# Kernel tuning notes

Measured on AMD Instinct MI355X. Metric: run time of the kernel, lower is better.

The kernel has to match this reference:

```python
import jax, jax.numpy as jnp
import numpy as np

D_MODEL = 1024
NUM_HEADS = 16
HEAD_DIM = D_MODEL // NUM_HEADS
D_FF = 4096
BATCH = 4
SEQ = 2048
LN_EPS = 1e-6
NEG_INF = -1e10


def setup_inputs() -> dict:
    key = jax.random.key(0)
    ks = jax.random.split(key, 8)
    def lin_init(k, fan_in, fan_out):
        # flax default: lecun_normal kernel, zeros bias
        w = jax.random.normal(k, (fan_in, fan_out), jnp.float32) / np.sqrt(fan_in)
        b = jnp.zeros((fan_out,), jnp.float32)
        return w, b
    x = jax.random.normal(ks[0], (BATCH, SEQ, D_MODEL), jnp.float32)
    w_qkv, b_qkv = lin_init(ks[1], D_MODEL, 3 * D_MODEL)
    w_out, b_out = lin_init(ks[2], D_MODEL, D_MODEL)
    w_fc1, b_fc1 = lin_init(ks[3], D_MODEL, D_FF)
    w_fc2, b_fc2 = lin_init(ks[4], D_FF, D_MODEL)
    ln1_scale = jnp.ones((D_MODEL,), jnp.float32)
    ln1_bias = jnp.zeros((D_MODEL,), jnp.float32)
    ln2_scale = jnp.ones((D_MODEL,), jnp.float32)
    ln2_bias = jnp.zeros((D_MODEL,), jnp.float32)
    return {
        'x': x,
        'w_qkv': w_qkv, 'b_qkv': b_qkv,
        'w_out': w_out, 'b_out': b_out,
        'w_fc1': w_fc1, 'b_fc1': b_fc1,
        'w_fc2': w_fc2, 'b_fc2': b_fc2,
        'ln1_scale': ln1_scale, 'ln1_bias': ln1_bias,
        'ln2_scale': ln2_scale, 'ln2_bias': ln2_bias,
    }


def _layernorm(x, scale, bias):
    mu = jnp.mean(x, axis=-1, keepdims=True)
    var = jnp.mean(jnp.square(x - mu), axis=-1, keepdims=True)
    return (x - mu) * jax.lax.rsqrt(var + LN_EPS) * scale + bias


def _attention(x, w_qkv, b_qkv, w_out, b_out):
    B, S, _ = x.shape
    qkv = x @ w_qkv + b_qkv                      # [B,S,3*D]
    qkv = qkv.reshape(B, S, 3, NUM_HEADS, HEAD_DIM)
    q, k, v = qkv[:, :, 0], qkv[:, :, 1], qkv[:, :, 2]   # [B,S,H,D]
    q = q.transpose(0, 2, 1, 3)                  # [B,H,S,D]
    k = k.transpose(0, 2, 1, 3)
    v = v.transpose(0, 2, 1, 3)
    scores = jnp.einsum('bhqd,bhkd->bhqk', q, k) / np.sqrt(HEAD_DIM)
    causal = jnp.tril(jnp.ones((S, S), bool))[None, None]
    scores = jnp.where(causal, scores, NEG_INF)
    attn = jax.nn.softmax(scores, axis=-1)
    out = jnp.einsum('bhqk,bhkd->bhqd', attn, v)  # [B,H,S,D]
    out = out.transpose(0, 2, 1, 3).reshape(B, S, D_MODEL)
    return out @ w_out + b_out


def _mlp(x, w_fc1, b_fc1, w_fc2, b_fc2):
    h = jax.nn.gelu(x @ w_fc1 + b_fc1)  # approximate (tanh) gelu, matching nnx.gelu default
    return h @ w_fc2 + b_fc2


def reference(x, w_qkv, b_qkv, w_out, b_out, w_fc1, b_fc1, w_fc2, b_fc2,
              ln1_scale, ln1_bias, ln2_scale, ln2_bias):
    x = x + _attention(_layernorm(x, ln1_scale, ln1_bias), w_qkv, b_qkv, w_out, b_out)
    x = x + _mlp(_layernorm(x, ln2_scale, ln2_bias), w_fc1, b_fc1, w_fc2, b_fc2)
    return x
```

## Files before the change

### kernel.cpp

```cpp
#include <hip/hip_runtime.h>

typedef unsigned short u16;
typedef unsigned int u32;
typedef __bf16 bf16x8 __attribute__((ext_vector_type(8)));
typedef float f32x4 __attribute__((ext_vector_type(4)));

constexpr int SEQ = 2048;

__device__ __forceinline__ float bf2f(u16 u) {
    u32 x = ((u32)u) << 16;
    return __builtin_bit_cast(float, x);
}
__device__ __forceinline__ u16 f2bf(float f) {
    u32 u = __builtin_bit_cast(u32, f);
    u32 r = u + 0x7fffu + ((u >> 16) & 1u);
    return (u16)(r >> 16);
}
__device__ __forceinline__ u32 cvt_pk_bf16(float a, float b) {
    u32 d;
    asm("v_cvt_pk_bf16_f32 %0, %1, %2" : "=v"(d) : "v"(a), "v"(b));
    return d;
}
__device__ __forceinline__ bf16x8 ld_frag(const u16* p) {
    uint4 u = *(const uint4*)p;
    return __builtin_bit_cast(bf16x8, u);
}
__device__ __forceinline__ float gelu_f(float x) {
    float u = 0.7978845608028654f * (x + 0.044715f * x * x * x);
    float e = exp2f(u * 2.885390081777927f);
    float t = 1.f - 2.f / (1.f + e);
    return 0.5f * x * (1.f + t);
}
__device__ __forceinline__ bool probe_f32(const u32* p) { return (p[0] & 0xFFFFu) == 0u; }

__device__ __forceinline__ void load_lds16(const u16* g, u16* l) {
    __builtin_amdgcn_global_load_lds(
        (const __attribute__((address_space(1))) void*)g,
        (__attribute__((address_space(3))) void*)l, 16, 0, 0);
}

__global__ __launch_bounds__(256) void convert_to_bf16(const void* __restrict__ in, long long off,
                                                       u16* __restrict__ out, int n,
                                                       const u32* __restrict__ probe) {
    const bool f32 = probe_f32(probe);
    int i = (blockIdx.x * 256 + threadIdx.x) * 4;
    if (i >= n) return;
    if (f32) {
        const float4 v = *(const float4*)((const float*)in + off + i);
        uint2 o;
        o.x = (u32)f2bf(v.x) | ((u32)f2bf(v.y) << 16);
        o.y = (u32)f2bf(v.z) | ((u32)f2bf(v.w) << 16);
        *(uint2*)(out + i) = o;
    } else {
        *(uint2*)(out + i) = *(const uint2*)((const u16*)in + off + i);
    }
}

__global__ __launch_bounds__(256) void finalize_out(const u16* __restrict__ in, void* __restrict__ outv,
                                                    long long off, int n, const u32* __restrict__ probe) {
    const bool f32 = probe_f32(probe);
    int i = (blockIdx.x * 256 + threadIdx.x) * 4;
    if (i >= n) return;
    uint2 v = *(const uint2*)(in + i);
    if (f32) {
        float4 o;
        o.x = bf2f((u16)(v.x & 0xffffu));
        o.y = bf2f((u16)(v.x >> 16));
        o.z = bf2f((u16)(v.y & 0xffffu));
        o.w = bf2f((u16)(v.y >> 16));
        *(float4*)((float*)outv + off + i) = o;
    } else {
        *(uint2*)((u16*)outv + off + i) = v;
    }
}

__global__ __launch_bounds__(256) void transpose_any(const void* __restrict__ in,
                                                     u16* __restrict__ out,
                                                     int K, int N, const u32* __restrict__ probe) {
    const bool f32 = probe_f32(probe);
    __shared__ u16 tile[32][33];
    int tx = threadIdx.x & 31, ty = threadIdx.x >> 5;
    int k0 = blockIdx.y * 32, n0 = blockIdx.x * 32;
    for (int i = 0; i < 32; i += 8) {
        size_t idx = (size_t)(k0 + ty + i) * N + n0 + tx;
        tile[ty + i][tx] = f32 ? f2bf(((const float*)in)[idx]) : ((const u16*)in)[idx];
    }
    __syncthreads();
    for (int i = 0; i < 32; i += 8)
        out[(size_t)(n0 + ty + i) * K + k0 + tx] = tile[tx][ty + i];
}

__global__ __launch_bounds__(256) void fused_cvt_ln(const void* __restrict__ xraw, long long off,
                                                    const u16* __restrict__ sc,
                                                    const u16* __restrict__ bi,
                                                    u16* __restrict__ xbf,
                                                    u16* __restrict__ xn,
                                                    const u32* __restrict__ probe) {
    const bool f32 = probe_f32(probe);
    int row = blockIdx.x;
    int tid = threadIdx.x;
    float v[4];
    if (f32) {
        const float4 q = *(const float4*)((const float*)xraw + off + (size_t)row * 1024 + tid * 4);
        v[0] = q.x; v[1] = q.y; v[2] = q.z; v[3] = q.w;
    } else {
        uint2 u = *(const uint2*)((const u16*)xraw + off + (size_t)row * 1024 + tid * 4);
        v[0] = bf2f((u16)(u.x & 0xffffu)); v[1] = bf2f((u16)(u.x >> 16));
        v[2] = bf2f((u16)(u.y & 0xffffu)); v[3] = bf2f((u16)(u.y >> 16));
    }
    {
        uint2 c;
        c.x = (u32)f2bf(v[0]) | ((u32)f2bf(v[1]) << 16);
        c.y = (u32)f2bf(v[2]) | ((u32)f2bf(v[3]) << 16);
        *(uint2*)(xbf + (size_t)row * 1024 + tid * 4) = c;
    }
    float s1 = 0.f, s2 = 0.f;
    for (int i = 0; i < 4; i++) { s1 += v[i]; s2 += v[i] * v[i]; }
    for (int off2 = 32; off2 >= 1; off2 >>= 1) {
        s1 += __shfl_xor(s1, off2, 64);
        s2 += __shfl_xor(s2, off2, 64);
    }
    __shared__ float red[8];
    int wave = tid >> 6, lane = tid & 63;
    if (lane == 0) { red[wave] = s1; red[4 + wave] = s2; }
    __syncthreads();
    s1 = red[0] + red[1] + red[2] + red[3];
    s2 = red[4] + red[5] + red[6] + red[7];
    float mean = s1 * (1.f / 1024.f);
    float var = s2 * (1.f / 1024.f) - mean * mean;
    float rstd = rsqrtf(var + 1e-6f);
    int c = tid * 4;
    float y0 = (v[0] - mean) * rstd * bf2f(sc[c + 0]) + bf2f(bi[c + 0]);
    float y1 = (v[1] - mean) * rstd * bf2f(sc[c + 1]) + bf2f(bi[c + 1]);
    float y2 = (v[2] - mean) * rstd * bf2f(sc[c + 2]) + bf2f(bi[c + 2]);
    float y3 = (v[3] - mean) * rstd * bf2f(sc[c + 3]) + bf2f(bi[c + 3]);
    uint2 ov;
    ov.x = (u32)f2bf(y0) | ((u32)f2bf(y1) << 16);
    ov.y = (u32)f2bf(y2) | ((u32)f2bf(y3) << 16);
    *(uint2*)(xn + (size_t)row * 1024 + tid * 4) = ov;
}

__global__ __launch_bounds__(256) void layernorm_k(const u16* __restrict__ x,
                                                   const u16* __restrict__ sc,
                                                   const u16* __restrict__ bi,
                                                   u16* __restrict__ out) {
    int row = blockIdx.x;
    int tid = threadIdx.x;
    const u16* xr = x + (size_t)row * 1024;
    uint2 u = *(const uint2*)(xr + tid * 4);
    float v[4];
    v[0] = bf2f((u16)(u.x & 0xffffu));
    v[1] = bf2f((u16)(u.x >> 16));
    v[2] = bf2f((u16)(u.y & 0xffffu));
    v[3] = bf2f((u16)(u.y >> 16));
    float s1 = 0.f, s2 = 0.f;
    for (int i = 0; i < 4; i++) { s1 += v[i]; s2 += v[i] * v[i]; }
    for (int off = 32; off >= 1; off >>= 1) {
        s1 += __shfl_xor(s1, off, 64);
        s2 += __shfl_xor(s2, off, 64);
    }
    __shared__ float red[8];
    int wave = tid >> 6, lane = tid & 63;
    if (lane == 0) { red[wave] = s1; red[4 + wave] = s2; }
    __syncthreads();
    s1 = red[0] + red[1] + red[2] + red[3];
    s2 = red[4] + red[5] + red[6] + red[7];
    float mean = s1 * (1.f / 1024.f);
    float var = s2 * (1.f / 1024.f) - mean * mean;
    float rstd = rsqrtf(var + 1e-6f);
    u32 o0, o1;
    {
        int c = tid * 4;
        float y0 = (v[0] - mean) * rstd * bf2f(sc[c + 0]) + bf2f(bi[c + 0]);
        float y1 = (v[1] - mean) * rstd * bf2f(sc[c + 1]) + bf2f(bi[c + 1]);
        float y2 = (v[2] - mean) * rstd * bf2f(sc[c + 2]) + bf2f(bi[c + 2]);
        float y3 = (v[3] - mean) * rstd * bf2f(sc[c + 3]) + bf2f(bi[c + 3]);
        o0 = (u32)f2bf(y0) | ((u32)f2bf(y1) << 16);
        o1 = (u32)f2bf(y2) | ((u32)f2bf(y3) << 16);
    }
    uint2 ov; ov.x = o0; ov.y = o1;
    *(uint2*)(out + (size_t)row * 1024 + tid * 4) = ov;
}

__device__ __forceinline__ void gemm_core(const u16* __restrict__ A, const u16* __restrict__ Bt,
                                          int K, int bm, int bn,
                                          u16* lA, u16* lB, f32x4 acc[4][4]) {
    const int tid = threadIdx.x, lane = tid & 63, wave = tid >> 6;
    const int wr = (wave >> 1) * 64, wc = (wave & 1) * 64;
    const int g = lane >> 4, l15 = lane & 15;
    const int srow = wave * 32 + (lane >> 3);
    const int gslot = (lane & 7) ^ (lane >> 3);
    const u16* gA = A + (size_t)(bm + srow) * K + gslot * 8;
    const u16* gB = Bt + (size_t)(bn + srow) * K + gslot * 8;
    u16* lAb = lA + wave * 2048;
    u16* lBb = lB + wave * 2048;
    const int sw = (l15 & 7);

    for (int kk = 0; kk < K; kk += 64) {
        __syncthreads();
#pragma unroll
        for (int q = 0; q < 4; q++) {
            load_lds16(gA + kk + q * 8 * K, lAb + q * 512);
            load_lds16(gB + kk + q * 8 * K, lBb + q * 512);
        }
        __syncthreads();
#pragma unroll
        for (int kh = 0; kh < 2; kh++) {
            bf16x8 af[4], bfr[4];
#pragma unroll
            for (int i = 0; i < 4; i++)
                af[i] = ld_frag(lA + (wr + i * 16 + l15) * 64 + (((kh * 4 + g) ^ sw) * 8));
#pragma unroll
            for (int j = 0; j < 4; j++)
                bfr[j] = ld_frag(lB + (wc + j * 16 + l15) * 64 + (((kh * 4 + g) ^ sw) * 8));
#pragma unroll
            for (int i = 0; i < 4; i++)
#pragma unroll
                for (int j = 0; j < 4; j++)
                    acc[i][j] = __builtin_amdgcn_mfma_f32_16x16x32_bf16(bfr[j], af[i], acc[i][j], 0, 0, 0);
        }
    }
}

__global__ __launch_bounds__(256) void gemm_bt(const u16* __restrict__ A,
                                               const u16* __restrict__ Bt,
                                               const u16* __restrict__ bias,
                                               const u16* __restrict__ res,
                                               u16* __restrict__ out,
                                               int M, int N, int K, int epi) {
    __shared__ __align__(16) u16 lA[128 * 64];
    __shared__ __align__(16) u16 lB[128 * 64];
    const int tid = threadIdx.x, lane = tid & 63, wave = tid >> 6;
    const int wr = (wave >> 1) * 64, wc = (wave & 1) * 64;
    const int g = lane >> 4, l15 = lane & 15;
    const int bm = blockIdx.y * 128, bn = blockIdx.x * 128;

    f32x4 acc[4][4];
    f32x4 zero = {0.f, 0.f, 0.f, 0.f};
    for (int i = 0; i < 4; i++)
        for (int j = 0; j < 4; j++) acc[i][j] = zero;

    gemm_core(A, Bt, K, bm, bn, lA, lB, acc);

    for (int j = 0; j < 4; j++) {
        const int gn0 = bn + wc + j * 16 + g * 4;
        const uint2 bv2 = *(const uint2*)(bias + gn0);
        const float b0 = bf2f((u16)(bv2.x & 0xffffu)), b1 = bf2f((u16)(bv2.x >> 16));
        const float b2 = bf2f((u16)(bv2.y & 0xffffu)), b3 = bf2f((u16)(bv2.y >> 16));
        for (int i = 0; i < 4; i++) {
            const int gm = bm + wr + i * 16 + l15;
            float v0 = acc[i][j][0] + b0, v1 = acc[i][j][1] + b1;
            float v2 = acc[i][j][2] + b2, v3 = acc[i][j][3] + b3;
            if (epi == 1) {
                const uint2 rv = *(const uint2*)(res + (size_t)gm * N + gn0);
                v0 += bf2f((u16)(rv.x & 0xffffu)); v1 += bf2f((u16)(rv.x >> 16));
                v2 += bf2f((u16)(rv.y & 0xffffu)); v3 += bf2f((u16)(rv.y >> 16));
            } else if (epi == 2) {
                v0 = gelu_f(v0); v1 = gelu_f(v1); v2 = gelu_f(v2); v3 = gelu_f(v3);
            }
            ushort4 o4;
            o4.x = f2bf(v0); o4.y = f2bf(v1); o4.z = f2bf(v2); o4.w = f2bf(v3);
            *(ushort4*)(out + (size_t)gm * N + gn0) = o4;
        }
    }
}

__global__ __launch_bounds__(256) void gemm_qkv(const u16* __restrict__ A,
                                                const u16* __restrict__ Bt,
                                                const u16* __restrict__ bias,
                                                u16* __restrict__ Qg,
                                                u16* __restrict__ Kg,
                                                u16* __restrict__ VTg,
                                                int K) {
    __shared__ __align__(16) u16 lA[128 * 64];
    __shared__ __align__(16) u16 lB[128 * 64];
    const int tid = threadIdx.x, lane = tid & 63, wave = tid >> 6;
    const int wr = (wave >> 1) * 64, wc = (wave & 1) * 64;
    const int g = lane >> 4, l15 = lane & 15;
    const int bm = blockIdx.y * 128, bn = blockIdx.x * 128;
    const float QSCALE = 0.18033688011112042f;

    f32x4 acc[4][4];
    f32x4 zero = {0.f, 0.f, 0.f, 0.f};
    for (int i = 0; i < 4; i++)
        for (int j = 0; j < 4; j++) acc[i][j] = zero;

    gemm_core(A, Bt, K, bm, bn, lA, lB, acc);

    for (int j = 0; j < 4; j++) {
        const int gn0 = bn + wc + j * 16 + g * 4;
        const int which = gn0 >> 10;
        const int hh = (gn0 >> 6) & 15, d0 = gn0 & 63;
        const uint2 bv2 = *(const uint2*)(bias + gn0);
        const float b0 = bf2f((u16)(bv2.x & 0xffffu)), b1 = bf2f((u16)(bv2.x >> 16));
        const float b2 = bf2f((u16)(bv2.y & 0xffffu)), b3 = bf2f((u16)(bv2.y >> 16));
        for (int i = 0; i < 4; i++) {
            const int s0 = bm + wr + i * 16 + l15;
            const int b = s0 >> 11, srel = s0 & 2047;
            const int bh = b * 16 + hh;
            const float v0 = acc[i][j][0] + b0, v1 = acc[i][j][1] + b1;
            const float v2 = acc[i][j][2] + b2, v3 = acc[i][j][3] + b3;
            if (which == 0) {
                ushort4 o4;
                o4.x = f2bf(v0 * QSCALE); o4.y = f2bf(v1 * QSCALE);
                o4.z = f2bf(v2 * QSCALE); o4.w = f2bf(v3 * QSCALE);
                *(ushort4*)(Qg + ((size_t)bh * SEQ + srel) * 64 + d0) = o4;
            } else if (which == 1) {
                ushort4 o4;
                o4.x = f2bf(v0); o4.y = f2bf(v1); o4.z = f2bf(v2); o4.w = f2bf(v3);
                *(ushort4*)(Kg + ((size_t)bh * SEQ + srel) * 64 + d0) = o4;
            } else {
                VTg[((size_t)bh * 64 + d0 + 0) * SEQ + srel] = f2bf(v0);
                VTg[((size_t)bh * 64 + d0 + 1) * SEQ + srel] = f2bf(v1);
                VTg[((size_t)bh * 64 + d0 + 2) * SEQ + srel] = f2bf(v2);
                VTg[((size_t)bh * 64 + d0 + 3) * SEQ + srel] = f2bf(v3);
            }
        }
    }
}

__device__ __forceinline__ void stage_kv(const u16* Kbh, const u16* Vbh, int kv0,
                                         u16* bK, u16* bV, int lane, int wave) {
    const int r = lane >> 3;
    const int gs = ((lane & 7) ^ r) * 8;
#pragma unroll
    for (int q = 0; q < 2; q++) {
        const int row = q * 32 + wave * 8 + r;
        load_lds16(Kbh + (size_t)(kv0 + row) * 64 + gs, bK + q * 2048 + wave * 512 + lane * 8);
        load_lds16(Vbh + (size_t)row * SEQ + kv0 + gs, bV + q * 2048 + wave * 512 + lane * 8);
    }
}

__global__ __launch_bounds__(256) void flash_attn6(const u16* __restrict__ Qg,
                                                   const u16* __restrict__ Kg,
                                                   const u16* __restrict__ VTg,
                                                   u16* __restrict__ attn) {
    __shared__ __align__(16) u16 lK[2][64 * 64];
    __shared__ __align__(16) u16 lVt[2][64 * 64];
    __shared__ __align__(16) u16 lP[4 * 32 * 72];

    const int bh = blockIdx.y;
    const int tid = threadIdx.x, lane = tid & 63, wave = tid >> 6;
    const int g = lane >> 4, l15 = lane & 15;
    const float MASKV = -3.0e4f;

    const u16* Qbh = Qg + (size_t)bh * SEQ * 64;
    const u16* Kbh = Kg + (size_t)bh * SEQ * 64;
    const u16* Vbh = VTg + (size_t)bh * 64 * SEQ;
    u16* myP = lP + wave * 32 * 72;
    const int b = bh >> 4, h = bh & 15;
    const f32x4 zero = {0.f, 0.f, 0.f, 0.f};
    const int sw = (l15 & 7);

    for (int ph = 0; ph < 2; ph++) {
        const int ti = ph ? blockIdx.x : (15 - blockIdx.x);
        const int q0 = ti * 128;
        const int qw = q0 + wave * 32;
        const int nfull = q0 >> 6;
        const int nt = nfull + 2;

        bf16x8 qf[2][2];
#pragma unroll
        for (int mi = 0; mi < 2; mi++)
#pragma unroll
            for (int kh = 0; kh < 2; kh++)
                qf[mi][kh] = ld_frag(Qbh + (size_t)(qw + mi * 16 + l15) * 64 + kh * 32 + g * 8);

        float l_[2] = {0.f, 0.f};
        f32x4 o[2][4];
        for (int mi = 0; mi < 2; mi++)
            for (int nj = 0; nj < 4; nj++) o[mi][nj] = zero;

        __syncthreads();
        stage_kv(Kbh, Vbh, 0, lK[0], lVt[0], lane, wave);

        for (int t = 0; t < nt; t++) {
            __syncthreads();
            if (t + 1 < nt)
                stage_kv(Kbh, Vbh, (t + 1) * 64, lK[(t + 1) & 1], lVt[(t + 1) & 1], lane, wave);
            const u16* bK = lK[t & 1];
            const u16* bV = lVt[t & 1];
            const bool diag = (t >= nfull);
            const int kv0 = t * 64;

            f32x4 sc[4][2];
#pragma unroll
            for (int ki = 0; ki < 4; ki++)
                for (int mi = 0; mi < 2; mi++) sc[ki][mi] = zero;
#pragma unroll
            for (int kh = 0; kh < 2; kh++) {
                bf16x8 kf[4];
#pragma unroll
                for (int ki = 0; ki < 4; ki++)
                    kf[ki] = ld_frag(bK + (ki * 16 + l15) * 64 + (((kh * 4 + g) ^ sw) * 8));
#pragma unroll
                for (int ki = 0; ki < 4; ki++)
#pragma unroll
                    for (int mi = 0; mi < 2; mi++)
                        sc[ki][mi] = __builtin_amdgcn_mfma_f32_16x16x32_bf16(kf[ki], qf[mi][kh], sc[ki][mi], 0, 0, 0);
            }

#pragma unroll
            for (int mi = 0; mi < 2; mi++) {
                const int qrow = qw + mi * 16 + l15;
                u16* pr = myP + (mi * 16 + l15) * 72 + g * 4;
                float lacc = 0.f;
#pragma unroll
                for (int ki = 0; ki < 4; ki++) {
                    const int kvb = kv0 + ki * 16 + g * 4;
                    float v0 = sc[ki][mi][0], v1 = sc[ki][mi][1];
                    float v2 = sc[ki][mi][2], v3 = sc[ki][mi][3];
                    if (diag) {
                        if (kvb + 0 > qrow) v0 = MASKV;
                        if (kvb + 1 > qrow) v1 = MASKV;
                        if (kvb + 2 > qrow) v2 = MASKV;
                        if (kvb + 3 > qrow) v3 = MASKV;
                    }
                    const float e0 = exp2f(v0), e1 = exp2f(v1);
                    const float e2 = exp2f(v2), e3 = exp2f(v3);
                    lacc += (e0 + e1) + (e2 + e3);
                    uint2 pw;
                    pw.x = cvt_pk_bf16(e0, e1);
                    pw.y = cvt_pk_bf16(e2, e3);
                    *(uint2*)(pr + ki * 16) = pw;
                }
                l_[mi] += lacc;
            }

#pragma unroll
            for (int ks = 0; ks < 2; ks++) {
                bf16x8 pa[2], vb[4];
#pragma unroll
                for (int mi = 0; mi < 2; mi++)
                    pa[mi] = ld_frag(myP + (mi * 16 + l15) * 72 + ks * 32 + g * 8);
#pragma unroll
                for (int nj = 0; nj < 4; nj++)
                    vb[nj] = ld_frag(bV + (nj * 16 + l15) * 64 + (((ks * 4 + g) ^ sw) * 8));
#pragma unroll
                for (int mi = 0; mi < 2; mi++)
#pragma unroll
                    for (int nj = 0; nj < 4; nj++)
                        o[mi][nj] = __builtin_amdgcn_mfma_f32_16x16x32_bf16(pa[mi], vb[nj], o[mi][nj], 0, 0, 0);
            }
        }

#pragma unroll
        for (int mi = 0; mi < 2; mi++) {
            float ls = l_[mi];
            ls += __shfl_xor(ls, 16, 64);
            ls += __shfl_xor(ls, 32, 64);
#pragma unroll
            for (int r = 0; r < 4; r++) {
                const float inv = 1.f / __shfl(ls, g * 4 + r, 64);
                const int row = qw + mi * 16 + g * 4 + r;
                const size_t orow = ((size_t)b * SEQ + row) * 1024 + h * 64;
                for (int nj = 0; nj < 4; nj++)
                    attn[orow + nj * 16 + l15] = f2bf(o[mi][nj][r] * inv);
            }
        }
    }
}

extern "C" void kernel_launch(void* const* d_in, const int* in_sizes, int n_in,
                              void* d_out, int out_size, void* d_ws, size_t ws_size,
                              hipStream_t stream) {
    const u32* probe = (const u32*)d_in[9];
    char* ws = (char*)d_ws;
    const size_t MB = 1048576;
    auto T = [&](size_t mb) { return (u16*)(ws + mb * MB); };
    auto conv = [&](const void* src, long long off, u16* dst, int n) {
        convert_to_bf16<<<(n / 4 + 255) / 256, 256, 0, stream>>>(src, off, dst, n, probe);
    };

    if (ws_size >= 160 * MB) {
        u16* xn1 = T(0), *Qg = T(16), *Kg = T(32), *VTg = T(48), *hbuf = T(0);
        u16* attn = T(64), *xn2 = T(64), *xbf = T(80), *resid1 = T(96), *outbf = T(112);
        u16* wTq = T(128), *wTo = T(134), *wT1 = T(136), *wT2 = T(144), *vecs = T(152);
        u16 *bqkvC = vecs, *boutC = vecs + 3072, *bfc1C = vecs + 4096, *bfc2C = vecs + 8192;
        u16 *ln1sC = vecs + 9216, *ln1bC = vecs + 10240, *ln2sC = vecs + 11264, *ln2bC = vecs + 12288;
        conv(d_in[2], 0, bqkvC, 3072); conv(d_in[4], 0, boutC, 1024);
        conv(d_in[6], 0, bfc1C, 4096); conv(d_in[8], 0, bfc2C, 1024);
        conv(d_in[9], 0, ln1sC, 1024); conv(d_in[10], 0, ln1bC, 1024);
        conv(d_in[11], 0, ln2sC, 1024); conv(d_in[12], 0, ln2bC, 1024);
        transpose_any<<<dim3(96, 32), 256, 0, stream>>>(d_in[1], wTq, 1024, 3072, probe);
        transpose_any<<<dim3(32, 32), 256, 0, stream>>>(d_in[3], wTo, 1024, 1024, probe);
        transpose_any<<<dim3(128, 32), 256, 0, stream>>>(d_in[5], wT1, 1024, 4096, probe);
        transpose_any<<<dim3(32, 128), 256, 0, stream>>>(d_in[7], wT2, 4096, 1024, probe);
        fused_cvt_ln<<<8192, 256, 0, stream>>>(d_in[0], 0, ln1sC, ln1bC, xbf, xn1, probe);
        gemm_qkv<<<dim3(24, 64), 256, 0, stream>>>(xn1, wTq, bqkvC, Qg, Kg, VTg, 1024);
        flash_attn6<<<dim3(8, 64), 256, 0, stream>>>(Qg, Kg, VTg, attn);
        gemm_bt<<<dim3(8, 64), 256, 0, stream>>>(attn, wTo, boutC, xbf, resid1, 8192, 1024, 1024, 1);
        layernorm_k<<<8192, 256, 0, stream>>>(resid1, ln2sC, ln2bC, xn2);
        gemm_bt<<<dim3(32, 64), 256, 0, stream>>>(xn2, wT1, bfc1C, nullptr, hbuf, 8192, 4096, 1024, 2);
        gemm_bt<<<dim3(8, 64), 256, 0, stream>>>(hbuf, wT2, bfc2C, resid1, outbf, 8192, 1024, 4096, 1);
        finalize_out<<<8192, 256, 0, stream>>>(outbf, d_out, 0, 8388608, probe);
    } else {
        u16* vecs = T(0);
        u16 *bqkvC = vecs, *boutC = vecs + 3072, *bfc1C = vecs + 4096, *bfc2C = vecs + 8192;
        u16 *ln1sC = vecs + 9216, *ln1bC = vecs + 10240, *ln2sC = vecs + 11264, *ln2bC = vecs + 12288;
        u16* wTq = T(1), *wTo = T(7), *wT1 = T(9), *wT2 = T(17);
        u16* xbf = T(25), *xn = T(29), *Qg = T(33), *Kg = T(37), *VTg = T(41);
        u16* attn_b = T(45), *resid_b = T(49), *h_b = T(53);
        conv(d_in[2], 0, bqkvC, 3072); conv(d_in[4], 0, boutC, 1024);
        conv(d_in[6], 0, bfc1C, 4096); conv(d_in[8], 0, bfc2C, 1024);
        conv(d_in[9], 0, ln1sC, 1024); conv(d_in[10], 0, ln1bC, 1024);
        conv(d_in[11], 0, ln2sC, 1024); conv(d_in[12], 0, ln2bC, 1024);
        transpose_any<<<dim3(96, 32), 256, 0, stream>>>(d_in[1], wTq, 1024, 3072, probe);
        transpose_any<<<dim3(32, 32), 256, 0, stream>>>(d_in[3], wTo, 1024, 1024, probe);
        transpose_any<<<dim3(128, 32), 256, 0, stream>>>(d_in[5], wT1, 1024, 4096, probe);
        transpose_any<<<dim3(32, 128), 256, 0, stream>>>(d_in[7], wT2, 4096, 1024, probe);
        for (int b = 0; b < 4; b++) {
            const long long ro = (long long)b * 2048 * 1024;
            fused_cvt_ln<<<2048, 256, 0, stream>>>(d_in[0], ro, ln1sC, ln1bC, xbf, xn, probe);
            gemm_qkv<<<dim3(24, 16), 256, 0, stream>>>(xn, wTq, bqkvC, Qg, Kg, VTg, 1024);
            flash_attn6<<<dim3(8, 16), 256, 0, stream>>>(Qg, Kg, VTg, attn_b);
            gemm_bt<<<dim3(8, 16), 256, 0, stream>>>(attn_b, wTo, boutC, xbf, resid_b, 2048, 1024, 1024, 1);
            layernorm_k<<<2048, 256, 0, stream>>>(resid_b, ln2sC, ln2bC, xn);
            for (int c = 0; c < 2; c++) {
                u16* xnc = xn + (size_t)c * 1024 * 1024;
                u16* resc = resid_b + (size_t)c * 1024 * 1024;
                u16* outc = xbf + (size_t)c * 1024 * 1024;
                gemm_bt<<<dim3(32, 8), 256, 0, stream>>>(xnc, wT1, bfc1C, nullptr, h_b, 1024, 4096, 1024, 2);
                gemm_bt<<<dim3(8, 8), 256, 0, stream>>>(h_b, wT2, bfc2C, resc, outc, 1024, 1024, 4096, 1);
                finalize_out<<<1024, 256, 0, stream>>>(outc, d_out, ro + c * 1048576, 1048576, probe);
            }
        }
    }
}
```

Before: 542.9 us.

## Double-buffer GEMM LDS tiles, remap blocks across XCDs, fuse output conversion

Changes the GEMM core to a double-buffered LDS pipeline: the next K tile is loaded while the current one is multiplied, leaving one barrier per iteration instead of two. Adds an XCD-aware block remapping to the GEMMs and flash attention so neighbouring tiles share an L2. Fuses the final f32/bf16 output conversion into the FC2 epilogue, removing the finalize kernel and one extra pass over the output. Epilogue stores now use packed bf16 conversion instructions. LDS use per block doubles, which may lower occupancy.

```diff
diff --git a/kernel.cpp b/kernel.cpp
--- a/kernel.cpp
+++ b/kernel.cpp
@@ -37,6 +37,15 @@
     __builtin_amdgcn_global_load_lds(
         (const __attribute__((address_space(1))) void*)g,
         (__attribute__((address_space(3))) void*)l, 16, 0, 0);
+}
+
+__device__ __forceinline__ void xcd_map(int& bx, int& by) {
+    const int gx = gridDim.x;
+    const int n = gx * gridDim.y;
+    const int orig = blockIdx.y * gx + blockIdx.x;
+    const int id = (orig & 7) * (n >> 3) + (orig >> 3);
+    bx = id % gx;
+    by = id / gx;
 }
 
 __global__ __launch_bounds__(256) void convert_to_bf16(const void* __restrict__ in, long long off,
@@ -53,24 +62,6 @@
         *(uint2*)(out + i) = o;
     } else {
         *(uint2*)(out + i) = *(const uint2*)((const u16*)in + off + i);
-    }
-}
-
-__global__ __launch_bounds__(256) void finalize_out(const u16* __restrict__ in, void* __restrict__ outv,
-                                                    long long off, int n, const u32* __restrict__ probe) {
-    const bool f32 = probe_f32(probe);
-    int i = (blockIdx.x * 256 + threadIdx.x) * 4;
-    if (i >= n) return;
-    uint2 v = *(const uint2*)(in + i);
-    if (f32) {
-        float4 o;
-        o.x = bf2f((u16)(v.x & 0xffffu));
-        o.y = bf2f((u16)(v.x >> 16));
-        o.z = bf2f((u16)(v.y & 0xffffu));
-        o.w = bf2f((u16)(v.y >> 16));
-        *(float4*)((float*)outv + off + i) = o;
-    } else {
-        *(uint2*)((u16*)outv + off + i) = v;
     }
 }
 
@@ -192,27 +183,44 @@
     const int gslot = (lane & 7) ^ (lane >> 3);
     const u16* gA = A + (size_t)(bm + srow) * K + gslot * 8;
     const u16* gB = Bt + (size_t)(bn + srow) * K + gslot * 8;
-    u16* lAb = lA + wave * 2048;
-    u16* lBb = lB + wave * 2048;
     const int sw = (l15 & 7);
-
-    for (int kk = 0; kk < K; kk += 64) {
+    const int nt = K >> 6;
+
+    {
+        u16* dA = lA + wave * 2048;
+        u16* dB = lB + wave * 2048;
+#pragma unroll
+        for (int q = 0; q < 4; q++) {
+            load_lds16(gA + q * 8 * K, dA + q * 512);
+            load_lds16(gB + q * 8 * K, dB + q * 512);
+        }
+    }
+
+    for (int t = 0; t < nt; t++) {
+        const int cur = (t & 1) * 8192;
         __syncthreads();
-#pragma unroll
-        for (int q = 0; q < 4; q++) {
-            load_lds16(gA + kk + q * 8 * K, lAb + q * 512);
-            load_lds16(gB + kk + q * 8 * K, lBb + q * 512);
-        }
-        __syncthreads();
+        if (t + 1 < nt) {
+            const int nxt = ((t + 1) & 1) * 8192;
+            const int kk = (t + 1) * 64;
+            u16* dA = lA + nxt + wave * 2048;
+            u16* dB = lB + nxt + wave * 2048;
+#pragma unroll
+            for (int q = 0; q < 4; q++) {
+                load_lds16(gA + kk + q * 8 * K, dA + q * 512);
+                load_lds16(gB + kk + q * 8 * K, dB + q * 512);
+            }
+        }
+        const u16* cA = lA + cur;
+        const u16* cB = lB + cur;
 #pragma unroll
         for (int kh = 0; kh < 2; kh++) {
             bf16x8 af[4], bfr[4];
 #pragma unroll
             for (int i = 0; i < 4; i++)
-                af[i] = ld_frag(lA + (wr + i * 16 + l15) * 64 + (((kh * 4 + g) ^ sw) * 8));
+                af[i] = ld_frag(cA + (wr + i * 16 + l15) * 64 + (((kh * 4 + g) ^ sw) * 8));
 #pragma unroll
             for (int j = 0; j < 4; j++)
-                bfr[j] = ld_frag(lB + (wc + j * 16 + l15) * 64 + (((kh * 4 + g) ^ sw) * 8));
+                bfr[j] = ld_frag(cB + (wc + j * 16 + l15) * 64 + (((kh * 4 + g) ^ sw) * 8));
 #pragma unroll
             for (int i = 0; i < 4; i++)
 #pragma unroll
@@ -226,14 +234,17 @@
                                                const u16* __restrict__ Bt,
                                                const u16* __restrict__ bias,
                                                const u16* __restrict__ res,
-                                               u16* __restrict__ out,
-                                               int M, int N, int K, int epi) {
-    __shared__ __align__(16) u16 lA[128 * 64];
-    __shared__ __align__(16) u16 lB[128 * 64];
+                                               void* __restrict__ out,
+                                               int M, int N, int K, int epi,
+                                               long long ooff, const u32* __restrict__ probe) {
+    __shared__ __align__(16) u16 lA[2 * 128 * 64];
+    __shared__ __align__(16) u16 lB[2 * 128 * 64];
     const int tid = threadIdx.x, lane = tid & 63, wave = tid >> 6;
     const int wr = (wave >> 1) * 64, wc = (wave & 1) * 64;
     const int g = lane >> 4, l15 = lane & 15;
-    const int bm = blockIdx.y * 128, bn = blockIdx.x * 128;
+    int bxi, byi;
+    xcd_map(bxi, byi);
+    const int bm = byi * 128, bn = bxi * 128;
 
     f32x4 acc[4][4];
     f32x4 zero = {0.f, 0.f, 0.f, 0.f};
@@ -242,6 +253,7 @@
 
     gemm_core(A, Bt, K, bm, bn, lA, lB, acc);
 
+    const bool of32 = (epi == 3) && probe_f32(probe);
     for (int j = 0; j < 4; j++) {
         const int gn0 = bn + wc + j * 16 + g * 4;
         const uint2 bv2 = *(const uint2*)(bias + gn0);
@@ -251,16 +263,27 @@
             const int gm = bm + wr + i * 16 + l15;
             float v0 = acc[i][j][0] + b0, v1 = acc[i][j][1] + b1;
             float v2 = acc[i][j][2] + b2, v3 = acc[i][j][3] + b3;
-            if (epi == 1) {
+            if (epi == 1 || epi == 3) {
                 const uint2 rv = *(const uint2*)(res + (size_t)gm * N + gn0);
                 v0 += bf2f((u16)(rv.x & 0xffffu)); v1 += bf2f((u16)(rv.x >> 16));
                 v2 += bf2f((u16)(rv.y & 0xffffu)); v3 += bf2f((u16)(rv.y >> 16));
             } else if (epi == 2) {
                 v0 = gelu_f(v0); v1 = gelu_f(v1); v2 = gelu_f(v2); v3 = gelu_f(v3);
             }
-            ushort4 o4;
-            o4.x = f2bf(v0); o4.y = f2bf(v1); o4.z = f2bf(v2); o4.w = f2bf(v3);
-            *(ushort4*)(out + (size_t)gm * N + gn0) = o4;
+            if (epi == 3) {
+                if (of32) {
+                    float4 o = {v0, v1, v2, v3};
+                    *(float4*)((float*)out + ooff + (size_t)gm * N + gn0) = o;
+                } else {
+                    uint2 o;
+                    o.x = cvt_pk_bf16(v0, v1); o.y = cvt_pk_bf16(v2, v3);
+                    *(uint2*)((u16*)out + ooff + (size_t)gm * N + gn0) = o;
+                }
+            } else {
+                uint2 o;
+                o.x = cvt_pk_bf16(v0, v1); o.y = cvt_pk_bf16(v2, v3);
+                *(uint2*)((u16*)out + (size_t)gm * N + gn0) = o;
+            }
         }
     }
 }
@@ -272,12 +295,14 @@
                                                 u16* __restrict__ Kg,
                                                 u16* __restrict__ VTg,
                                                 int K) {
-    __shared__ __align__(16) u16 lA[128 * 64];
-    __shared__ __align__(16) u16 lB[128 * 64];
+    __shared__ __align__(16) u16 lA[2 * 128 * 64];
+    __shared__ __align__(16) u16 lB[2 * 128 * 64];
     const int tid = threadIdx.x, lane = tid & 63, wave = tid >> 6;
     const int wr = (wave >> 1) * 64, wc = (wave & 1) * 64;
     const int g = lane >> 4, l15 = lane & 15;
-    const int bm = blockIdx.y * 128, bn = blockIdx.x * 128;
+    int bxi, byi;
+    xcd_map(bxi, byi);
+    const int bm = byi * 128, bn = bxi * 128;
     const float QSCALE = 0.18033688011112042f;
 
     f32x4 acc[4][4];
@@ -301,14 +326,14 @@
             const float v0 = acc[i][j][0] + b0, v1 = acc[i][j][1] + b1;
             const float v2 = acc[i][j][2] + b2, v3 = acc[i][j][3] + b3;
             if (which == 0) {
-                ushort4 o4;
-                o4.x = f2bf(v0 * QSCALE); o4.y = f2bf(v1 * QSCALE);
-                o4.z = f2bf(v2 * QSCALE); o4.w = f2bf(v3 * QSCALE);
-                *(ushort4*)(Qg + ((size_t)bh * SEQ + srel) * 64 + d0) = o4;
+                uint2 o;
+                o.x = cvt_pk_bf16(v0 * QSCALE, v1 * QSCALE);
+                o.y = cvt_pk_bf16(v2 * QSCALE, v3 * QSCALE);
+                *(uint2*)(Qg + ((size_t)bh * SEQ + srel) * 64 + d0) = o;
             } else if (which == 1) {
-                ushort4 o4;
-                o4.x = f2bf(v0); o4.y = f2bf(v1); o4.z = f2bf(v2); o4.w = f2bf(v3);
-                *(ushort4*)(Kg + ((size_t)bh * SEQ + srel) * 64 + d0) = o4;
+                uint2 o;
+                o.x = cvt_pk_bf16(v0, v1); o.y = cvt_pk_bf16(v2, v3);
+                *(uint2*)(Kg + ((size_t)bh * SEQ + srel) * 64 + d0) = o;
             } else {
                 VTg[((size_t)bh * 64 + d0 + 0) * SEQ + srel] = f2bf(v0);
                 VTg[((size_t)bh * 64 + d0 + 1) * SEQ + srel] = f2bf(v1);
@@ -339,7 +364,9 @@
     __shared__ __align__(16) u16 lVt[2][64 * 64];
     __shared__ __align__(16) u16 lP[4 * 32 * 72];
 
-    const int bh = blockIdx.y;
+    int bxi, byi;
+    xcd_map(bxi, byi);
+    const int bh = byi;
     const int tid = threadIdx.x, lane = tid & 63, wave = tid >> 6;
     const int g = lane >> 4, l15 = lane & 15;
     const float MASKV = -3.0e4f;
@@ -353,7 +380,7 @@
     const int sw = (l15 & 7);
 
     for (int ph = 0; ph < 2; ph++) {
-        const int ti = ph ? blockIdx.x : (15 - blockIdx.x);
+        const int ti = ph ? bxi : (15 - bxi);
         const int q0 = ti * 128;
         const int qw = q0 + wave * 32;
         const int nfull = q0 >> 6;
@@ -474,7 +501,7 @@
 
     if (ws_size >= 160 * MB) {
         u16* xn1 = T(0), *Qg = T(16), *Kg = T(32), *VTg = T(48), *hbuf = T(0);
-        u16* attn = T(64), *xn2 = T(64), *xbf = T(80), *resid1 = T(96), *outbf = T(112);
+        u16* attn = T(64), *xn2 = T(64), *xbf = T(80), *resid1 = T(96);
         u16* wTq = T(128), *wTo = T(134), *wT1 = T(136), *wT2 = T(144), *vecs = T(152);
         u16 *bqkvC = vecs, *boutC = vecs + 3072, *bfc1C = vecs + 4096, *bfc2C = vecs + 8192;
         u16 *ln1sC = vecs + 9216, *ln1bC = vecs + 10240, *ln2sC = vecs + 11264, *ln2bC = vecs + 12288;
@@ -489,11 +516,10 @@
         fused_cvt_ln<<<8192, 256, 0, stream>>>(d_in[0], 0, ln1sC, ln1bC, xbf, xn1, probe);
         gemm_qkv<<<dim3(24, 64), 256, 0, stream>>>(xn1, wTq, bqkvC, Qg, Kg, VTg, 1024);
         flash_attn6<<<dim3(8, 64), 256, 0, stream>>>(Qg, Kg, VTg, attn);
-        gemm_bt<<<dim3(8, 64), 256, 0, stream>>>(attn, wTo, boutC, xbf, resid1, 8192, 1024, 1024, 1);
+        gemm_bt<<<dim3(8, 64), 256, 0, stream>>>(attn, wTo, boutC, xbf, resid1, 8192, 1024, 1024, 1, 0, probe);
         layernorm_k<<<8192, 256, 0, stream>>>(resid1, ln2sC, ln2bC, xn2);
-        gemm_bt<<<dim3(32, 64), 256, 0, stream>>>(xn2, wT1, bfc1C, nullptr, hbuf, 8192, 4096, 1024, 2);
-        gemm_bt<<<dim3(8, 64), 256, 0, stream>>>(hbuf, wT2, bfc2C, resid1, outbf, 8192, 1024, 4096, 1);
-        finalize_out<<<8192, 256, 0, stream>>>(outbf, d_out, 0, 8388608, probe);
+        gemm_bt<<<dim3(32, 64), 256, 0, stream>>>(xn2, wT1, bfc1C, nullptr, hbuf, 8192, 4096, 1024, 2, 0, probe);
+        gemm_bt<<<dim3(8, 64), 256, 0, stream>>>(hbuf, wT2, bfc2C, resid1, d_out, 8192, 1024, 4096, 3, 0, probe);
     } else {
         u16* vecs = T(0);
         u16 *bqkvC = vecs, *boutC = vecs + 3072, *bfc1C = vecs + 4096, *bfc2C = vecs + 8192;
@@ -514,16 +540,14 @@
             fused_cvt_ln<<<2048, 256, 0, stream>>>(d_in[0], ro, ln1sC, ln1bC, xbf, xn, probe);
             gemm_qkv<<<dim3(24, 16), 256, 0, stream>>>(xn, wTq, bqkvC, Qg, Kg, VTg, 1024);
             flash_attn6<<<dim3(8, 16), 256, 0, stream>>>(Qg, Kg, VTg, attn_b);
-            gemm_bt<<<dim3(8, 16), 256, 0, stream>>>(attn_b, wTo, boutC, xbf, resid_b, 2048, 1024, 1024, 1);
+            gemm_bt<<<dim3(8, 16), 256, 0, stream>>>(attn_b, wTo, boutC, xbf, resid_b, 2048, 1024, 1024, 1, 0, probe);
             layernorm_k<<<2048, 256, 0, stream>>>(resid_b, ln2sC, ln2bC, xn);
             for (int c = 0; c < 2; c++) {
                 u16* xnc = xn + (size_t)c * 1024 * 1024;
                 u16* resc = resid_b + (size_t)c * 1024 * 1024;
-                u16* outc = xbf + (size_t)c * 1024 * 1024;
-                gemm_bt<<<dim3(32, 8), 256, 0, stream>>>(xnc, wT1, bfc1C, nullptr, h_b, 1024, 4096, 1024, 2);
-                gemm_bt<<<dim3(8, 8), 256, 0, stream>>>(h_b, wT2, bfc2C, resc, outc, 1024, 1024, 4096, 1);
-                finalize_out<<<1024, 256, 0, stream>>>(outc, d_out, ro + c * 1048576, 1048576, probe);
-            }
-        }
-    }
-}
+                gemm_bt<<<dim3(32, 8), 256, 0, stream>>>(xnc, wT1, bfc1C, nullptr, h_b, 1024, 4096, 1024, 2, 0, probe);
+                gemm_bt<<<dim3(8, 8), 256, 0, stream>>>(h_b, wT2, bfc2C, resc, d_out, 1024, 1024, 4096, 3, ro + (long long)c * 1048576, probe);
+            }
+        }
+    }
+}
```

New measurement: 539.5 us, median of 2. Within noise of the previous version (-0.6%).
